# Kernel tuning notes

Hardware: AMD Instinct MI355X
Metric: run time of the kernel (lower is better)

Reference implementation:

```python
import jax, jax.numpy as jnp
import numpy as np
from functools import partial

H = 51  # hidden size hard-coded in the module


def _lstm_cell(x, h, c, W_ih, b_ih, W_hh, b_hh):
    # PyTorch LSTMCell gate order: i, f, g, o stacked along dim 0 of W (4H rows)
    gates = x @ W_ih.T + b_ih + h @ W_hh.T + b_hh  # [B, 4H]
    i, f, g, o = jnp.split(gates, 4, axis=-1)
    i = jax.nn.sigmoid(i)
    f = jax.nn.sigmoid(f)
    g = jnp.tanh(g)
    o = jax.nn.sigmoid(o)
    c_new = f * c + i * g
    h_new = o * jnp.tanh(c_new)
    return h_new, c_new


def setup_inputs() -> dict:
    key = jax.random.key(0)
    ks = jax.random.split(key, 11)
    B, T = 2048, 512
    bound = 1.0 / np.sqrt(H)  # torch LSTMCell/Linear default init: U(-1/sqrt(H), 1/sqrt(H))
    u = lambda k, shape: jax.random.uniform(k, shape, jnp.float32, -bound, bound)
    return {
        "x": jax.random.normal(ks[0], (B, T), dtype=jnp.float32),
        "future": 0,
        "W_ih1": u(ks[1], (4 * H, 1)),
        "b_ih1": u(ks[2], (4 * H,)),
        "W_hh1": u(ks[3], (4 * H, H)),
        "b_hh1": u(ks[4], (4 * H,)),
        "W_ih2": u(ks[5], (4 * H, H)),
        "b_ih2": u(ks[6], (4 * H,)),
        "W_hh2": u(ks[7], (4 * H, H)),
        "b_hh2": u(ks[8], (4 * H,)),
        "fc_w": u(ks[9], (1, H)),
        "fc_b": u(ks[10], (1,)),
    }


def reference(x, future, W_ih1, b_ih1, W_hh1, b_hh1,
              W_ih2, b_ih2, W_hh2, b_hh2, fc_w, fc_b):
    B = x.shape[0]
    z = jnp.zeros((B, H), dtype=x.dtype)

    def cell_stack(x_t, carry):
        h1, c1, h2, c2 = carry
        h1, c1 = _lstm_cell(x_t, h1, c1, W_ih1, b_ih1, W_hh1, b_hh1)
        h2, c2 = _lstm_cell(h1, h2, c2, W_ih2, b_ih2, W_hh2, b_hh2)
        out = h2 @ fc_w.T + fc_b  # [B, 1]
        return (h1, c1, h2, c2), out

    def step(carry, x_t):
        return cell_stack(x_t, carry)

    xs = jnp.swapaxes(x, 0, 1)[:, :, None]  # [T, B, 1]
    carry, outs = jax.lax.scan(step, (z, z, z, z), xs)  # outs: [T, B, 1]
    outputs = jnp.swapaxes(outs[:, :, 0], 0, 1)  # [B, T]

    if future > 0:
        last = outs[-1]  # [B, 1]

        def fstep(c, _):
            inner, out = c
            inner, out = cell_stack(out, inner)
            return (inner, out), out

        _, fouts = jax.lax.scan(fstep, (carry, last), None, length=future)
        outputs = jnp.concatenate([outputs, jnp.swapaxes(fouts[:, :, 0], 0, 1)], axis=1)

    return outputs
```

## Files before the change

kernel.cpp:

```cpp
#include <hip/hip_runtime.h>

#define HID   51
#define T_LEN 512
#define BT    8
#define NTH   832

#define X_OFF   0
#define OUT_OFF 4128
#define H1_OFF  8256
#define H2_OFF  9280

typedef _Float16 h8 __attribute__((ext_vector_type(8)));
typedef float    f4 __attribute__((ext_vector_type(4)));

__device__ __forceinline__ float fast_rcp(float x) { return __builtin_amdgcn_rcpf(x); }
__device__ __forceinline__ float sigm(float x) { return fast_rcp(1.0f + __expf(-x)); }
__device__ __forceinline__ float tanh_f(float x) {
    x = fminf(15.0f, fmaxf(-15.0f, x));
    float e = __expf(2.0f * x);
    return (e - 1.0f) * fast_rcp(e + 1.0f);
}
__device__ __forceinline__ float tanh_nc(float x) {
    float e = __expf(2.0f * x);
    return (e - 1.0f) * fast_rcp(e + 1.0f);
}

__device__ __forceinline__ float dpp_ror8(float v) {
    int t = __builtin_amdgcn_update_dpp(0, __float_as_int(v), 0x128, 0xf, 0xf, true);
    return __int_as_float(t);
}

__device__ __forceinline__ h8 cvt_frag1(const float* p) {
    float4 a = *(const float4*)p;
    float4 b = *(const float4*)(p + 4);
    h8 h;
    h[0] = (_Float16)a.x; h[1] = (_Float16)a.y; h[2] = (_Float16)a.z; h[3] = (_Float16)a.w;
    h[4] = (_Float16)b.x; h[5] = (_Float16)b.y; h[6] = (_Float16)b.z; h[7] = (_Float16)b.w;
    return h;
}

__device__ __forceinline__ float gate_update(const float G[4], float& c) {
    float iv = sigm(G[0]), fv = sigm(G[1]), gv = tanh_nc(G[2]), ov = sigm(G[3]);
    c = fv * c + iv * gv;
    return ov * tanh_f(c);
}

#define MFMA16(A, B, C) __builtin_amdgcn_mfma_f32_16x16x32_f16((A), (B), (C), 0, 0, 0)

__global__ __launch_bounds__(NTH)
void lstm_seq_kernel(const float* __restrict__ x,
                     const float* __restrict__ W_ih1, const float* __restrict__ b_ih1,
                     const float* __restrict__ W_hh1, const float* __restrict__ b_hh1,
                     const float* __restrict__ W_ih2, const float* __restrict__ b_ih2,
                     const float* __restrict__ W_hh2, const float* __restrict__ b_hh2,
                     const float* __restrict__ fc_w,  const float* __restrict__ fc_b,
                     float* __restrict__ out)
{
    __shared__ __align__(16) float sb[13312];

    const int tid   = threadIdx.x;
    const int b0    = blockIdx.x * BT;
    const int w     = tid >> 6;
    const int lane  = tid & 63;
    const int row16 = lane & 15;
    const int q4    = lane >> 4;
    const int col   = row16;

    h8 a1f[2];
    h8 a2f[4];

    for (int i = tid; i < 208 * 64; i += NTH) {
        int rp = i >> 6, k = i & 63;
        int j = rp >> 2, g = rp & 3;
        sb[i] = (j < HID && k < HID) ? W_hh1[(g * HID + j) * HID + k] : 0.0f;
    }
    __syncthreads();
    #pragma unroll
    for (int kt = 0; kt < 2; ++kt)
        a1f[kt] = cvt_frag1(sb + (w * 16 + row16) * 64 + kt * 32 + q4 * 8);
    __syncthreads();

    for (int i = tid; i < 208 * 64; i += NTH) {
        int rp = i >> 6, k = i & 63;
        int j = rp >> 2, g = rp & 3;
        sb[i] = (j < HID && k < HID) ? W_ih2[(g * HID + j) * HID + k] : 0.0f;
    }
    __syncthreads();
    #pragma unroll
    for (int kt = 0; kt < 2; ++kt)
        a2f[kt] = cvt_frag1(sb + (w * 16 + row16) * 64 + kt * 32 + q4 * 8);
    __syncthreads();

    for (int i = tid; i < 208 * 64; i += NTH) {
        int rp = i >> 6, k = i & 63;
        int j = rp >> 2, g = rp & 3;
        float v = 0.0f;
        if (k < HID) {
            if (j < HID)        v = W_hh2[(g * HID + j) * HID + k];
            else if (rp == 204) v = fc_w[k];
        }
        sb[i] = v;
    }
    __syncthreads();
    #pragma unroll
    for (int kt = 0; kt < 2; ++kt)
        a2f[kt + 2] = cvt_frag1(sb + (w * 16 + row16) * 64 + kt * 32 + q4 * 8);
    __syncthreads();

    const int jq = 4 * w + q4;
    f4 bi1, bi2;
    float wr1[4];
    #pragma unroll
    for (int g = 0; g < 4; ++g) {
        bi1[g] = (jq < HID) ? (b_ih1[g * HID + jq] + b_hh1[g * HID + jq]) : 0.f;
        bi2[g] = (jq < HID) ? (b_ih2[g * HID + jq] + b_hh2[g * HID + jq]) : 0.f;
        wr1[g] = (jq < HID) ? W_ih1[g * HID + jq] : 0.f;
    }
    const bool lay1 = (col < 8);
    const int  bsel = col & 7;
    const bool val  = (jq < HID);
    const int offh  = (lay1 ? H1_OFF : H2_OFF) * 2
                    + (jq >> 5) * 512 + ((((jq & 31) >> 3) << 4) + bsel) * 8 + (jq & 7);

    float* xl   = sb + X_OFF;
    float* outl = sb + OUT_OFF;
    for (int i = tid; i < BT * 516; i += NTH) {
        int b = i / 516, t = i - 516 * b;
        xl[i] = (t < T_LEN) ? x[(size_t)(b0 + b) * T_LEN + t] : 0.0f;
    }
    for (int i = tid; i < 2048; i += NTH) sb[H1_OFF + i] = 0.0f;

    float c = 0.f;
    const float fcb = fc_b[0];
    const bool outlane = (w == 12) && (q4 == 3) && (col < 8);
    const float* xp  = xl + bsel * 516;
    const float* rA0 = sb + H1_OFF + lane * 4;
    const float* rB0 = sb + H2_OFF + lane * 4;
    _Float16* hwp = (_Float16*)sb + offh;
    __syncthreads();

    if (lay1) {
        float xv = xp[0];
        float G[4];
        #pragma unroll
        for (int g = 0; g < 4; ++g) G[g] = bi1[g] + wr1[g] * xv;
        float hv = gate_update(G, c);
        if (val) hwp[0] = (_Float16)hv;
    }
    __syncthreads();

    auto body = [&](int i, int p) {
        float xv = xp[i + 1];
        const float* rA = rA0 + p * 512;
        const float* rB = rB0 + p * 512;
        h8 bh0 = *(const h8*)(rA);       h8 bh1 = *(const h8*)(rA + 256);
        h8 ch2 = *(const h8*)(rB);       h8 ch3 = *(const h8*)(rB + 256);

        f4 s = bi1;
        s = MFMA16(a1f[0], bh0, s);
        s = MFMA16(a1f[1], bh1, s);
        f4 u = bi2;
        u = MFMA16(a2f[0], bh0, u);
        u = MFMA16(a2f[1], bh1, u);
        u = MFMA16(a2f[2], ch2, u);
        u = MFMA16(a2f[3], ch3, u);

        float fcv = u[0];
        float G[4];
        #pragma unroll
        for (int g = 0; g < 4; ++g) {
            float ur = dpp_ror8(u[g]);
            G[g] = lay1 ? (s[g] + wr1[g] * xv) : ur;
        }
        float hv = gate_update(G, c);
        if (val) hwp[(p ^ 1) * 1024] = (_Float16)hv;
        if (outlane && i >= 1) outl[col * 516 + (i - 1)] = fcb + fcv;
        __syncthreads();
    };
    for (int i = 0; i < T_LEN; i += 2) {
        body(i, 0);
        body(i + 1, 1);
    }
    body(T_LEN, 0);

    for (int i = tid; i < BT * T_LEN; i += NTH) {
        int b = i >> 9, tt = i & (T_LEN - 1);
        out[(size_t)(b0 + b) * T_LEN + tt] = outl[b * 516 + tt];
    }
}

extern "C" void kernel_launch(void* const* d_in, const int* in_sizes, int n_in,
                              void* d_out, int out_size, void* d_ws, size_t ws_size,
                              hipStream_t stream) {
    const float* x      = (const float*)d_in[0];
    const float* W_ih1  = (const float*)d_in[2];
    const float* b_ih1v = (const float*)d_in[3];
    const float* W_hh1  = (const float*)d_in[4];
    const float* b_hh1v = (const float*)d_in[5];
    const float* W_ih2  = (const float*)d_in[6];
    const float* b_ih2v = (const float*)d_in[7];
    const float* W_hh2  = (const float*)d_in[8];
    const float* b_hh2v = (const float*)d_in[9];
    const float* fc_w   = (const float*)d_in[10];
    const float* fc_b   = (const float*)d_in[11];
    float* out = (float*)d_out;

    dim3 grid(2048 / BT);
    dim3 block(NTH);
    lstm_seq_kernel<<<grid, block, 0, stream>>>(x, W_ih1, b_ih1v, W_hh1, b_hh1v,
                                                W_ih2, b_ih2v, W_hh2, b_hh2v,
                                                fc_w, fc_b, out);
}
```

Baseline: 394.8 us.

## Split hidden-state buffers into two batch images with interleaved MFMA chains

```diff
diff --git a/kernel.cpp b/kernel.cpp
--- a/kernel.cpp
+++ b/kernel.cpp
@@ -5,10 +5,12 @@
 #define BT    8
 #define NTH   832
 
-#define X_OFF   0
-#define OUT_OFF 4128
-#define H1_OFF  8256
-#define H2_OFF  9280
+#define X_OFF    0
+#define OUT_OFF  4128
+#define HA1_OFF  8256
+#define HB1_OFF  9280
+#define HA2_OFF  10304
+#define HB2_OFF  11328
 
 typedef _Float16 h8 __attribute__((ext_vector_type(8)));
 typedef float    f4 __attribute__((ext_vector_type(4)));
@@ -117,9 +119,11 @@
         wr1[g] = (jq < HID) ? W_ih1[g * HID + jq] : 0.f;
     }
     const bool lay1 = (col < 8);
+    const bool strB = (col & 4) != 0;
     const int  bsel = col & 7;
     const bool val  = (jq < HID);
-    const int offh  = (lay1 ? H1_OFF : H2_OFF) * 2
+    const int  img  = lay1 ? (strB ? HB1_OFF : HA1_OFF) : (strB ? HB2_OFF : HA2_OFF);
+    const int  offh = img * 2
                     + (jq >> 5) * 512 + ((((jq & 31) >> 3) << 4) + bsel) * 8 + (jq & 7);
 
     float* xl   = sb + X_OFF;
@@ -128,14 +132,16 @@
         int b = i / 516, t = i - 516 * b;
         xl[i] = (t < T_LEN) ? x[(size_t)(b0 + b) * T_LEN + t] : 0.0f;
     }
-    for (int i = tid; i < 2048; i += NTH) sb[H1_OFF + i] = 0.0f;
+    for (int i = tid; i < 4096; i += NTH) sb[HA1_OFF + i] = 0.0f;
 
     float c = 0.f;
     const float fcb = fc_b[0];
     const bool outlane = (w == 12) && (q4 == 3) && (col < 8);
-    const float* xp  = xl + bsel * 516;
-    const float* rA0 = sb + H1_OFF + lane * 4;
-    const float* rB0 = sb + H2_OFF + lane * 4;
+    const float* xp   = xl + bsel * 516;
+    const float* rA1 = sb + HA1_OFF + lane * 4;
+    const float* rB1 = sb + HB1_OFF + lane * 4;
+    const float* rA2 = sb + HA2_OFF + lane * 4;
+    const float* rB2 = sb + HB2_OFF + lane * 4;
     _Float16* hwp = (_Float16*)sb + offh;
     __syncthreads();
 
@@ -151,26 +157,28 @@
 
     auto body = [&](int i, int p) {
         float xv = xp[i + 1];
-        const float* rA = rA0 + p * 512;
-        const float* rB = rB0 + p * 512;
-        h8 bh0 = *(const h8*)(rA);       h8 bh1 = *(const h8*)(rA + 256);
-        h8 ch2 = *(const h8*)(rB);       h8 ch3 = *(const h8*)(rB + 256);
-
-        f4 s = bi1;
-        s = MFMA16(a1f[0], bh0, s);
-        s = MFMA16(a1f[1], bh1, s);
-        f4 u = bi2;
-        u = MFMA16(a2f[0], bh0, u);
-        u = MFMA16(a2f[1], bh1, u);
-        u = MFMA16(a2f[2], ch2, u);
-        u = MFMA16(a2f[3], ch3, u);
-
-        float fcv = u[0];
+        h8 ah0 = *(const h8*)(rA1 + p * 512); h8 ah1 = *(const h8*)(rA1 + p * 512 + 256);
+        h8 ac2 = *(const h8*)(rA2 + p * 512); h8 ac3 = *(const h8*)(rA2 + p * 512 + 256);
+        h8 bh0 = *(const h8*)(rB1 + p * 512); h8 bh1 = *(const h8*)(rB1 + p * 512 + 256);
+        h8 bc2 = *(const h8*)(rB2 + p * 512); h8 bc3 = *(const h8*)(rB2 + p * 512 + 256);
+
+        f4 sA = bi1, sB = bi1, uA = bi2, uB = bi2;
+        sA = MFMA16(a1f[0], ah0, sA); sB = MFMA16(a1f[0], bh0, sB);
+        uA = MFMA16(a2f[0], ah0, uA); uB = MFMA16(a2f[0], bh0, uB);
+        sA = MFMA16(a1f[1], ah1, sA); sB = MFMA16(a1f[1], bh1, sB);
+        uA = MFMA16(a2f[1], ah1, uA); uB = MFMA16(a2f[1], bh1, uB);
+        uA = MFMA16(a2f[2], ac2, uA); uB = MFMA16(a2f[2], bc2, uB);
+        uA = MFMA16(a2f[3], ac3, uA); uB = MFMA16(a2f[3], bc3, uB);
+
+        float fcv = strB ? uB[0] : uA[0];
         float G[4];
         #pragma unroll
         for (int g = 0; g < 4; ++g) {
-            float ur = dpp_ror8(u[g]);
-            G[g] = lay1 ? (s[g] + wr1[g] * xv) : ur;
+            float sg  = strB ? sB[g] : sA[g];
+            float urA = dpp_ror8(uA[g]);
+            float urB = dpp_ror8(uB[g]);
+            float ug  = strB ? urB : urA;
+            G[g] = lay1 ? (sg + wr1[g] * xv) : ug;
         }
         float hv = gate_update(G, c);
         if (val) hwp[(p ^ 1) * 1024] = (_Float16)hv;
```

New measurement: 508.7 us. +28.8%, slower.
